# Optimization experiments

Measured on AMD Instinct MI355X. Metric: run time of the kernel, lower is better.

Reference implementation:

```python
import jax, jax.numpy as jnp
import numpy as np

B, T, D = 8, 2048, 128


def setup_inputs() -> dict:
    key = jax.random.key(0)
    kq, kk, kv = jax.random.split(key, 3)
    q = jax.random.normal(kq, (B, T, D), dtype=jnp.float32)
    k = jax.random.normal(kk, (B, T, D), dtype=jnp.float32)
    v = jax.random.normal(kv, (B, T, D), dtype=jnp.float32)
    # causal mask, broadcast over batch; 0 -> masked
    mask = jnp.tril(jnp.ones((T, T), dtype=jnp.int32))[None, :, :]
    mode = jnp.float32(0.5)  # learnable scalar parameter (init 0.5)
    return {"q": q, "k": k, "v": v, "mask": mask, "mode": mode}


def reference(q, k, v, mask, mode):
    scale = D ** (-0.5)
    # meson score: -(Q K^T) * scale
    meson = -jnp.einsum("btd,bsd->bts", q, k) * scale
    # baryon score: Q against K with feature dim rolled by 1
    k_perm = jnp.roll(k, shift=1, axis=-1)
    baryon = jnp.einsum("btd,bsd->bts", q, k_perm) * scale
    alpha = jax.nn.sigmoid(mode)
    attn = alpha * meson + (1.0 - alpha) * baryon
    attn = jnp.where(mask == 0, -jnp.inf, attn)
    attn = jax.nn.softmax(attn, axis=-1)
    return jnp.einsum("bts,bsd->btd", attn, v)
```

## Files before the change

kernel.cpp:

```cpp
#include <hip/hip_runtime.h>
#include <hip/hip_bf16.h>
#include <cstdint>
#include <cstddef>


typedef __attribute__((ext_vector_type(8))) short short8;
typedef __attribute__((ext_vector_type(4))) float f32x4;
typedef __attribute__((ext_vector_type(16))) float f32x16;
typedef __attribute__((ext_vector_type(4))) unsigned uint4v;

#define T_DIM 2048
#define D_DIM 128
#define B_DIM 8
#define SEGT 8
#define POSLOTS_PER_B 112
#define MLSLOTS_PER_B 144
#define LOG2E 1.4426950408889634f

__device__ __forceinline__ unsigned short f2bf(float f) {
  unsigned u = __builtin_bit_cast(unsigned, f);
  u += 0x7FFFu + ((u >> 16) & 1u);
  return (unsigned short)(u >> 16);
}
__device__ __forceinline__ float bf2f(unsigned short u) {
  return __uint_as_float(((unsigned)u) << 16);
}
__device__ __forceinline__ unsigned pack2bf(float a, float b) {
  return (unsigned)f2bf(a) | ((unsigned)f2bf(b) << 16);
}
__device__ __forceinline__ void gload_lds16(const void* g, void* l) {
  __builtin_amdgcn_global_load_lds(
      (const __attribute__((address_space(1))) unsigned int*)g,
      (__attribute__((address_space(3))) unsigned int*)l, 16, 0, 0);
}

__global__ __launch_bounds__(256) void prep_all(
    const float* __restrict__ q, const float* __restrict__ k, const float* __restrict__ v,
    const float* __restrict__ modep,
    unsigned short* __restrict__ qbf, unsigned short* __restrict__ kbf,
    unsigned short* __restrict__ vt)
{
  __shared__ unsigned short tile[64 * 136];
  const int b = blockIdx.x, s0 = blockIdx.y * 64;
  const int tid = threadIdx.x;
  const float alpha = 1.f / (1.f + __expf(-modep[0]));
  const float scale = 0.08838834764831845f;
  const float ca = -alpha * scale * LOG2E, cb = (1.f - alpha) * scale * LOG2E;

#pragma unroll
  for (int u = 0; u < 4; ++u) {
    int c = u * 256 + tid;
    int r = c >> 4, c8 = c & 15;
    size_t row = (size_t)b * T_DIM + s0 + r;
    float4 ka = *(const float4*)(k + row * D_DIM + c8 * 8);
    float4 kb2 = *(const float4*)(k + row * D_DIM + c8 * 8 + 4);
    short8 ko = { (short)f2bf(ka.x), (short)f2bf(ka.y), (short)f2bf(ka.z), (short)f2bf(ka.w),
                  (short)f2bf(kb2.x), (short)f2bf(kb2.y), (short)f2bf(kb2.z), (short)f2bf(kb2.w) };
    *(short8*)(kbf + row * D_DIM + c8 * 8) = ko;
    const float* qr = q + row * D_DIM;
    float e[9];
    float4 f0 = *(const float4*)(qr + c8 * 8);
    float4 f1 = *(const float4*)(qr + c8 * 8 + 4);
    e[0] = f0.x; e[1] = f0.y; e[2] = f0.z; e[3] = f0.w;
    e[4] = f1.x; e[5] = f1.y; e[6] = f1.z; e[7] = f1.w;
    e[8] = qr[(c8 * 8 + 8) & 127];
    short8 qo;
#pragma unroll
    for (int j = 0; j < 8; ++j) qo[j] = (short)f2bf(ca * e[j] + cb * e[j + 1]);
    *(short8*)(qbf + row * D_DIM + c8 * 8) = qo;
    float4 va = *(const float4*)(v + row * D_DIM + c8 * 8);
    float4 vb2 = *(const float4*)(v + row * D_DIM + c8 * 8 + 4);
    short8 vo = { (short)f2bf(va.x), (short)f2bf(va.y), (short)f2bf(va.z), (short)f2bf(va.w),
                  (short)f2bf(vb2.x), (short)f2bf(vb2.y), (short)f2bf(vb2.z), (short)f2bf(vb2.w) };
    *(short8*)(tile + r * 136 + c8 * 8) = vo;
  }
  __syncthreads();
#pragma unroll
  for (int u = 0; u < 8; ++u) {
    int c = u * 256 + tid;
    int d = c >> 4, sq = c & 15;
    ushort4 o = { tile[(sq * 4 + 0) * 136 + d], tile[(sq * 4 + 1) * 136 + d],
                  tile[(sq * 4 + 2) * 136 + d], tile[(sq * 4 + 3) * 136 + d] };
    *(ushort4*)(vt + ((size_t)b * D_DIM + d) * T_DIM + s0 + sq * 4) = o;
  }
}

__global__ __launch_bounds__(128, 2) void attn_kernel(
    const unsigned short* __restrict__ qbf, const unsigned short* __restrict__ kbf,
    const unsigned short* __restrict__ vt, float* __restrict__ out,
    unsigned short* __restrict__ po, float* __restrict__ ml)
{
  __shared__ uint4 smem4[2048];
  char* smem = (char*)smem4;
  const int tid = threadIdx.x;
  const int w = tid >> 6, lane = tid & 63;
  const int q32 = lane & 31, h = lane >> 5;
  const int b = blockIdx.x;
  const int c = 31 - (int)blockIdx.y;
  const int s = blockIdx.z;
  const int nt = 2 * c + 2;
  const int nseg = (c + 4) >> 2;
  if (s >= nseg) return;
  const int t0 = s * SEGT;
  const int t1 = min(nt, t0 + SEGT);
  const int qbw = c * 64 + w * 32;
  const int qg = qbw + q32;

  const unsigned short* kbase = kbf + (size_t)b * T_DIM * D_DIM;
  const unsigned short* vbase = vt + (size_t)b * D_DIM * T_DIM;

  short8 qf[8];
  {
    const unsigned short* qr = qbf + ((size_t)b * T_DIM + qg) * D_DIM;
#pragma unroll
    for (int j = 0; j < 8; ++j) qf[j] = *(const short8*)(qr + (2 * j + h) * 8);
  }

  f32x16 acc[4];
#pragma unroll
  for (int dt = 0; dt < 4; ++dt) acc[dt] = (f32x16)(0.f);
  float mrun = -1e30f, lsum = 0.f;

  auto stage = [&](int cur, int kt) {
    const int kv0 = kt * 32;
    char* kb = smem + cur * 8192;
    char* vb = smem + 16384 + cur * 8192;
#pragma unroll
    for (int u = 0; u < 4; ++u) {
      int s_loc = w * 16 + u * 4 + (lane >> 4);
      int slot = (lane & 15) ^ (s_loc & 15);
      gload_lds16(kbase + (size_t)(kv0 + s_loc) * D_DIM + slot * 8,
                  kb + w * 4096 + u * 1024);
    }
#pragma unroll
    for (int u = 0; u < 4; ++u) {
      int d_loc = w * 64 + u * 16 + (lane >> 2);
      int vslot = (lane & 3) ^ (d_loc & 3);
      gload_lds16(vbase + (size_t)d_loc * T_DIM + kv0 + vslot * 8,
                  vb + w * 4096 + u * 1024);
    }
  };

  stage(0, t0);
  __syncthreads();
  int cur = 0;

  for (int kt = t0; kt < t1; ++kt) {
    if (kt + 1 < t1) stage(cur ^ 1, kt + 1);
    const int kv0 = kt * 32;

    if (kv0 <= qbw + 31) {
      char* kb = smem + cur * 8192;
      char* vb = smem + 16384 + cur * 8192;

      f32x16 sj = (f32x16)(0.f);
#pragma unroll
      for (int j = 0; j < 8; ++j) {
        int r = q32;
        short8 kf = *(const short8*)(kb + r * 256 + (((2 * j + h) ^ (r & 15)) << 4));
        sj = __builtin_amdgcn_mfma_f32_32x32x16_bf16(kf, qf[j], sj, 0, 0, 0);
      }

      if (kv0 == qbw) {
#pragma unroll
        for (int r = 0; r < 16; ++r) {
          int kvg = kv0 + (r & 3) + 8 * (r >> 2) + 4 * h;
          if (kvg > qg) sj[r] = -1e30f;
        }
      }

      float lm = sj[0];
#pragma unroll
      for (int r = 1; r < 16; ++r) lm = fmaxf(lm, sj[r]);
      int ok = (lm <= mrun + 11.0f);
      if (!__all(ok)) {
        float tm = fmaxf(lm, __shfl_xor(lm, 32));
        float mnew = fmaxf(mrun, tm);
        float corr = exp2f(mrun - mnew);
        mrun = mnew;
        lsum *= corr;
#pragma unroll
        for (int dt = 0; dt < 4; ++dt) acc[dt] *= corr;
      }

      float ls = 0.f;
#pragma unroll
      for (int r = 0; r < 16; ++r) {
        float p = exp2f(sj[r] - mrun);
        sj[r] = p;
        ls += p;
      }
      lsum += ls;

      unsigned W[8];
#pragma unroll
      for (int t = 0; t < 8; ++t) W[t] = pack2bf(sj[2 * t], sj[2 * t + 1]);
      short8 pf[2];
#pragma unroll
      for (int j = 0; j < 2; ++j) {
        unsigned w0 = W[4 * j + 0], w1 = W[4 * j + 1];
        unsigned w2 = W[4 * j + 2], w3 = W[4 * j + 3];
        unsigned s0 = (unsigned)__shfl_xor((int)w0, 32);
        unsigned s1 = (unsigned)__shfl_xor((int)w1, 32);
        unsigned s2 = (unsigned)__shfl_xor((int)w2, 32);
        unsigned s3 = (unsigned)__shfl_xor((int)w3, 32);
        uint4v bw = { h ? s2 : w0, h ? s3 : w1, h ? w2 : s0, h ? w3 : s1 };
        pf[j] = __builtin_bit_cast(short8, bw);
      }

#pragma unroll
      for (int dt = 0; dt < 4; ++dt) {
        int d = dt * 32 + q32;
#pragma unroll
        for (int j = 0; j < 2; ++j) {
          short8 vf = *(const short8*)(vb + d * 64 + (((2 * j + h) ^ (d & 3)) << 4));
          acc[dt] = __builtin_amdgcn_mfma_f32_32x32x16_bf16(vf, pf[j], acc[dt], 0, 0, 0);
        }
      }
    }

    __syncthreads();
    cur ^= 1;
  }

  float lred = lsum + __shfl_xor(lsum, 32);

  if (nseg == 1) {
    float inv = 1.0f / lred;
    float* orow = out + ((size_t)b * T_DIM + qg) * D_DIM;
#pragma unroll
    for (int dt = 0; dt < 4; ++dt)
#pragma unroll
      for (int rg = 0; rg < 4; ++rg) {
        int d0 = dt * 32 + rg * 8 + 4 * h;
        f32x4 o = { acc[dt][4 * rg] * inv, acc[dt][4 * rg + 1] * inv,
                    acc[dt][4 * rg + 2] * inv, acc[dt][4 * rg + 3] * inv };
        *(f32x4*)(orow + d0) = o;
      }
  } else {
    int pofs = 0;
    for (int cc = 0; cc < c; ++cc) pofs += ((cc + 4) >> 2) - 1;
    if (s == 0) {
      float* orow = out + ((size_t)b * T_DIM + qg) * D_DIM;
#pragma unroll
      for (int dt = 0; dt < 4; ++dt)
#pragma unroll
        for (int rg = 0; rg < 4; ++rg) {
          int d0 = dt * 32 + rg * 8 + 4 * h;
          f32x4 o = { acc[dt][4 * rg], acc[dt][4 * rg + 1],
                      acc[dt][4 * rg + 2], acc[dt][4 * rg + 3] };
          *(f32x4*)(orow + d0) = o;
        }
    } else {
      unsigned short* prow = po + ((size_t)b * POSLOTS_PER_B + pofs + (s - 1)) * 8192 +
                             (w * 32 + q32) * 128;
#pragma unroll
      for (int dt = 0; dt < 4; ++dt)
#pragma unroll
        for (int rg = 0; rg < 4; ++rg) {
          int d0 = dt * 32 + rg * 8 + 4 * h;
          ushort4 o = { f2bf(acc[dt][4 * rg]), f2bf(acc[dt][4 * rg + 1]),
                        f2bf(acc[dt][4 * rg + 2]), f2bf(acc[dt][4 * rg + 3]) };
          *(ushort4*)(prow + d0) = o;
        }
    }
    if (h == 0) {
      const size_t mlslot = (size_t)b * MLSLOTS_PER_B + pofs + c + s;
      int rb = w * 32 + q32;
      ml[mlslot * 128 + rb] = mrun;
      ml[mlslot * 128 + 64 + rb] = lred;
    }
  }
}

__global__ __launch_bounds__(256) void combine_kernel(
    const unsigned short* __restrict__ po, const float* __restrict__ ml,
    float* __restrict__ out)
{
  const int tid = threadIdx.x;
  const int b = blockIdx.x;
  const int c = 4 + (int)blockIdx.y;
  const int nseg = (c + 4) >> 2;
  int pofs = 0;
  for (int cc = 0; cc < c; ++cc) pofs += ((cc + 4) >> 2) - 1;
  const size_t mlbase = (size_t)b * MLSLOTS_PER_B + pofs + c;
  const size_t pobase = (size_t)b * POSLOTS_PER_B + pofs;

  __shared__ float wgt[64][8];
  if (tid < 64) {
    float M = -1e30f;
    for (int s = 0; s < nseg; ++s)
      M = fmaxf(M, ml[(mlbase + s) * 128 + tid]);
    float L = 0.f;
    for (int s = 0; s < nseg; ++s) {
      float e = exp2f(ml[(mlbase + s) * 128 + tid] - M);
      wgt[tid][s] = e;
      L += e * ml[(mlbase + s) * 128 + 64 + tid];
    }
    float invL = 1.f / L;
    for (int s = 0; s < nseg; ++s) wgt[tid][s] *= invL;
  }
  __syncthreads();

#pragma unroll
  for (int it = 0; it < 4; ++it) {
    int vid = it * 256 + tid;
    int r = vid >> 4, ch = vid & 15;
    float* op = out + ((size_t)b * T_DIM + c * 64 + r) * D_DIM + ch * 8;
    float4 a0 = *(const float4*)op;
    float4 a1 = *(const float4*)(op + 4);
    float w0 = wgt[r][0];
    float o[8] = { w0 * a0.x, w0 * a0.y, w0 * a0.z, w0 * a0.w,
                   w0 * a1.x, w0 * a1.y, w0 * a1.z, w0 * a1.w };
    for (int s = 1; s < nseg; ++s) {
      short8 pv = *(const short8*)(po + (pobase + s - 1) * 8192 + r * 128 + ch * 8);
      float ws = wgt[r][s];
#pragma unroll
      for (int j = 0; j < 8; ++j) o[j] += ws * bf2f((unsigned short)pv[j]);
    }
    *(float4*)op = (float4){o[0], o[1], o[2], o[3]};
    *(float4*)(op + 4) = (float4){o[4], o[5], o[6], o[7]};
  }
}

extern "C" void kernel_launch(void* const* d_in, const int* in_sizes, int n_in,
                              void* d_out, int out_size, void* d_ws, size_t ws_size,
                              hipStream_t stream) {
  const float* q = (const float*)d_in[0];
  const float* k = (const float*)d_in[1];
  const float* v = (const float*)d_in[2];
  const float* mode = (const float*)d_in[4];
  float* out = (float*)d_out;

  char* ws = (char*)d_ws;
  unsigned short* qbf = (unsigned short*)(ws);
  unsigned short* kbf = (unsigned short*)(ws + 4194304);
  unsigned short* vtb = (unsigned short*)(ws + 8388608);
  unsigned short* po  = (unsigned short*)(ws + 12582912);
  float*          ml  = (float*)(ws + 27262976);

  prep_all<<<dim3(B_DIM, T_DIM / 64), 256, 0, stream>>>(q, k, v, mode, qbf, kbf, vtb);
  attn_kernel<<<dim3(B_DIM, 32, SEGT), 128, 0, stream>>>(qbf, kbf, vtb, out, po, ml);
  combine_kernel<<<dim3(B_DIM, 28), 256, 0, stream>>>(po, ml, out);
}
```

Measured before the change: 57.23 us.

## Assign one KV segment per wave with 32-row query tiles, dropping LDS staging

```diff
diff --git a/kernel.cpp b/kernel.cpp
--- a/kernel.cpp
+++ b/kernel.cpp
@@ -13,8 +13,8 @@
 #define D_DIM 128
 #define B_DIM 8
 #define SEGT 8
-#define POSLOTS_PER_B 112
-#define MLSLOTS_PER_B 144
+#define POSLOTS_PER_B 224
+#define MLSLOTS_PER_B 288
 #define LOG2E 1.4426950408889634f
 
 __device__ __forceinline__ unsigned short f2bf(float f) {
@@ -27,11 +27,6 @@
 }
 __device__ __forceinline__ unsigned pack2bf(float a, float b) {
   return (unsigned)f2bf(a) | ((unsigned)f2bf(b) << 16);
-}
-__device__ __forceinline__ void gload_lds16(const void* g, void* l) {
-  __builtin_amdgcn_global_load_lds(
-      (const __attribute__((address_space(1))) unsigned int*)g,
-      (__attribute__((address_space(3))) unsigned int*)l, 16, 0, 0);
 }
 
 __global__ __launch_bounds__(256) void prep_all(
@@ -85,26 +80,24 @@
   }
 }
 
-__global__ __launch_bounds__(128, 2) void attn_kernel(
+__global__ __launch_bounds__(256, 3) void attn_kernel(
     const unsigned short* __restrict__ qbf, const unsigned short* __restrict__ kbf,
     const unsigned short* __restrict__ vt, float* __restrict__ out,
     unsigned short* __restrict__ po, float* __restrict__ ml)
 {
-  __shared__ uint4 smem4[2048];
-  char* smem = (char*)smem4;
   const int tid = threadIdx.x;
   const int w = tid >> 6, lane = tid & 63;
   const int q32 = lane & 31, h = lane >> 5;
   const int b = blockIdx.x;
-  const int c = 31 - (int)blockIdx.y;
-  const int s = blockIdx.z;
-  const int nt = 2 * c + 2;
-  const int nseg = (c + 4) >> 2;
+  const int c = 63 - (int)blockIdx.y;
+  const int s = (int)blockIdx.z * 4 + w;
+  const int nt = c + 1;
+  const int nseg = (c + 8) >> 3;
   if (s >= nseg) return;
   const int t0 = s * SEGT;
   const int t1 = min(nt, t0 + SEGT);
-  const int qbw = c * 64 + w * 32;
-  const int qg = qbw + q32;
+  const int qb = c * 32;
+  const int qg = qb + q32;
 
   const unsigned short* kbase = kbf + (size_t)b * T_DIM * D_DIM;
   const unsigned short* vbase = vt + (size_t)b * D_DIM * T_DIM;
@@ -121,106 +114,73 @@
   for (int dt = 0; dt < 4; ++dt) acc[dt] = (f32x16)(0.f);
   float mrun = -1e30f, lsum = 0.f;
 
-  auto stage = [&](int cur, int kt) {
+  for (int kt = t0; kt < t1; ++kt) {
     const int kv0 = kt * 32;
-    char* kb = smem + cur * 8192;
-    char* vb = smem + 16384 + cur * 8192;
-#pragma unroll
-    for (int u = 0; u < 4; ++u) {
-      int s_loc = w * 16 + u * 4 + (lane >> 4);
-      int slot = (lane & 15) ^ (s_loc & 15);
-      gload_lds16(kbase + (size_t)(kv0 + s_loc) * D_DIM + slot * 8,
-                  kb + w * 4096 + u * 1024);
-    }
-#pragma unroll
-    for (int u = 0; u < 4; ++u) {
-      int d_loc = w * 64 + u * 16 + (lane >> 2);
-      int vslot = (lane & 3) ^ (d_loc & 3);
-      gload_lds16(vbase + (size_t)d_loc * T_DIM + kv0 + vslot * 8,
-                  vb + w * 4096 + u * 1024);
-    }
-  };
-
-  stage(0, t0);
-  __syncthreads();
-  int cur = 0;
-
-  for (int kt = t0; kt < t1; ++kt) {
-    if (kt + 1 < t1) stage(cur ^ 1, kt + 1);
-    const int kv0 = kt * 32;
-
-    if (kv0 <= qbw + 31) {
-      char* kb = smem + cur * 8192;
-      char* vb = smem + 16384 + cur * 8192;
-
-      f32x16 sj = (f32x16)(0.f);
-#pragma unroll
-      for (int j = 0; j < 8; ++j) {
-        int r = q32;
-        short8 kf = *(const short8*)(kb + r * 256 + (((2 * j + h) ^ (r & 15)) << 4));
-        sj = __builtin_amdgcn_mfma_f32_32x32x16_bf16(kf, qf[j], sj, 0, 0, 0);
+
+    const unsigned short* kr = kbase + (size_t)(kv0 + q32) * D_DIM;
+    f32x16 sj = (f32x16)(0.f);
+#pragma unroll
+    for (int j = 0; j < 8; ++j) {
+      short8 kf = *(const short8*)(kr + (2 * j + h) * 8);
+      sj = __builtin_amdgcn_mfma_f32_32x32x16_bf16(kf, qf[j], sj, 0, 0, 0);
+    }
+
+    if (kt == c) {
+#pragma unroll
+      for (int r = 0; r < 16; ++r) {
+        int kvg = kv0 + (r & 3) + 8 * (r >> 2) + 4 * h;
+        if (kvg > qg) sj[r] = -1e30f;
       }
-
-      if (kv0 == qbw) {
-#pragma unroll
-        for (int r = 0; r < 16; ++r) {
-          int kvg = kv0 + (r & 3) + 8 * (r >> 2) + 4 * h;
-          if (kvg > qg) sj[r] = -1e30f;
-        }
+    }
+
+    float lm = sj[0];
+#pragma unroll
+    for (int r = 1; r < 16; ++r) lm = fmaxf(lm, sj[r]);
+    int ok = (lm <= mrun + 11.0f);
+    if (!__all(ok)) {
+      float tm = fmaxf(lm, __shfl_xor(lm, 32));
+      float mnew = fmaxf(mrun, tm);
+      float corr = exp2f(mrun - mnew);
+      mrun = mnew;
+      lsum *= corr;
+#pragma unroll
+      for (int dt = 0; dt < 4; ++dt) acc[dt] *= corr;
+    }
+
+    float ls = 0.f;
+#pragma unroll
+    for (int r = 0; r < 16; ++r) {
+      float p = exp2f(sj[r] - mrun);
+      sj[r] = p;
+      ls += p;
+    }
+    lsum += ls;
+
+    unsigned W[8];
+#pragma unroll
+    for (int t = 0; t < 8; ++t) W[t] = pack2bf(sj[2 * t], sj[2 * t + 1]);
+    short8 pf[2];
+#pragma unroll
+    for (int j = 0; j < 2; ++j) {
+      unsigned w0 = W[4 * j + 0], w1 = W[4 * j + 1];
+      unsigned w2 = W[4 * j + 2], w3 = W[4 * j + 3];
+      unsigned s0 = (unsigned)__shfl_xor((int)w0, 32);
+      unsigned s1 = (unsigned)__shfl_xor((int)w1, 32);
+      unsigned s2 = (unsigned)__shfl_xor((int)w2, 32);
+      unsigned s3 = (unsigned)__shfl_xor((int)w3, 32);
+      uint4v bw = { h ? s2 : w0, h ? s3 : w1, h ? w2 : s0, h ? w3 : s1 };
+      pf[j] = __builtin_bit_cast(short8, bw);
+    }
+
+#pragma unroll
+    for (int dt = 0; dt < 4; ++dt) {
+      const unsigned short* vr = vbase + (size_t)(dt * 32 + q32) * T_DIM + kv0;
+#pragma unroll
+      for (int j = 0; j < 2; ++j) {
+        short8 vf = *(const short8*)(vr + (2 * j + h) * 8);
+        acc[dt] = __builtin_amdgcn_mfma_f32_32x32x16_bf16(vf, pf[j], acc[dt], 0, 0, 0);
       }
-
-      float lm = sj[0];
-#pragma unroll
-      for (int r = 1; r < 16; ++r) lm = fmaxf(lm, sj[r]);
-      int ok = (lm <= mrun + 11.0f);
-      if (!__all(ok)) {
-        float tm = fmaxf(lm, __shfl_xor(lm, 32));
-        float mnew = fmaxf(mrun, tm);
-        float corr = exp2f(mrun - mnew);
-        mrun = mnew;
-        lsum *= corr;
-#pragma unroll
-        for (int dt = 0; dt < 4; ++dt) acc[dt] *= corr;
-      }
-
-      float ls = 0.f;
-#pragma unroll
-      for (int r = 0; r < 16; ++r) {
-        float p = exp2f(sj[r] - mrun);
-        sj[r] = p;
-        ls += p;
-      }
-      lsum += ls;
-
-      unsigned W[8];
-#pragma unroll
-      for (int t = 0; t < 8; ++t) W[t] = pack2bf(sj[2 * t], sj[2 * t + 1]);
-      short8 pf[2];
-#pragma unroll
-      for (int j = 0; j < 2; ++j) {
-        unsigned w0 = W[4 * j + 0], w1 = W[4 * j + 1];
-        unsigned w2 = W[4 * j + 2], w3 = W[4 * j + 3];
-        unsigned s0 = (unsigned)__shfl_xor((int)w0, 32);
-        unsigned s1 = (unsigned)__shfl_xor((int)w1, 32);
-        unsigned s2 = (unsigned)__shfl_xor((int)w2, 32);
-        unsigned s3 = (unsigned)__shfl_xor((int)w3, 32);
-        uint4v bw = { h ? s2 : w0, h ? s3 : w1, h ? w2 : s0, h ? w3 : s1 };
-        pf[j] = __builtin_bit_cast(short8, bw);
-      }
-
-#pragma unroll
-      for (int dt = 0; dt < 4; ++dt) {
-        int d = dt * 32 + q32;
-#pragma unroll
-        for (int j = 0; j < 2; ++j) {
-          short8 vf = *(const short8*)(vb + d * 64 + (((2 * j + h) ^ (d & 3)) << 4));
-          acc[dt] = __builtin_amdgcn_mfma_f32_32x32x16_bf16(vf, pf[j], acc[dt], 0, 0, 0);
-        }
-      }
-    }
-
-    __syncthreads();
-    cur ^= 1;
+    }
   }
 
   float lred = lsum + __shfl_xor(lsum, 32);
@@ -239,7 +199,7 @@
       }
   } else {
     int pofs = 0;
-    for (int cc = 0; cc < c; ++cc) pofs += ((cc + 4) >> 2) - 1;
+    for (int cc = 0; cc < c; ++cc) pofs += ((cc + SEGT) >> 3) - 1;
     if (s == 0) {
       float* orow = out + ((size_t)b * T_DIM + qg) * D_DIM;
 #pragma unroll
@@ -252,8 +212,8 @@
           *(f32x4*)(orow + d0) = o;
         }
     } else {
-      unsigned short* prow = po + ((size_t)b * POSLOTS_PER_B + pofs + (s - 1)) * 8192 +
-                             (w * 32 + q32) * 128;
+      unsigned short* prow = po + ((size_t)b * POSLOTS_PER_B + pofs + (s - 1)) * 4096 +
+                             q32 * 128;
 #pragma unroll
       for (int dt = 0; dt < 4; ++dt)
 #pragma unroll
@@ -266,9 +226,8 @@
     }
     if (h == 0) {
       const size_t mlslot = (size_t)b * MLSLOTS_PER_B + pofs + c + s;
-      int rb = w * 32 + q32;
-      ml[mlslot * 128 + rb] = mrun;
-      ml[mlslot * 128 + 64 + rb] = lred;
+      ml[mlslot * 64 + q32] = mrun;
+      ml[mlslot * 64 + 32 + q32] = lred;
     }
   }
 }
@@ -279,23 +238,24 @@
 {
   const int tid = threadIdx.x;
   const int b = blockIdx.x;
-  const int c = 4 + (int)blockIdx.y;
-  const int nseg = (c + 4) >> 2;
+  const int c = SEGT + (int)blockIdx.y;
+  const int nt = c + 1;
+  const int nseg = (nt + SEGT - 1) >> 3;
   int pofs = 0;
-  for (int cc = 0; cc < c; ++cc) pofs += ((cc + 4) >> 2) - 1;
+  for (int cc = 0; cc < c; ++cc) pofs += ((cc + SEGT) >> 3) - 1;
   const size_t mlbase = (size_t)b * MLSLOTS_PER_B + pofs + c;
   const size_t pobase = (size_t)b * POSLOTS_PER_B + pofs;
 
-  __shared__ float wgt[64][8];
-  if (tid < 64) {
+  __shared__ float wgt[32][8];
+  if (tid < 32) {
     float M = -1e30f;
     for (int s = 0; s < nseg; ++s)
-      M = fmaxf(M, ml[(mlbase + s) * 128 + tid]);
+      M = fmaxf(M, ml[(mlbase + s) * 64 + tid]);
     float L = 0.f;
     for (int s = 0; s < nseg; ++s) {
-      float e = exp2f(ml[(mlbase + s) * 128 + tid] - M);
+      float e = exp2f(ml[(mlbase + s) * 64 + tid] - M);
       wgt[tid][s] = e;
-      L += e * ml[(mlbase + s) * 128 + 64 + tid];
+      L += e * ml[(mlbase + s) * 64 + 32 + tid];
     }
     float invL = 1.f / L;
     for (int s = 0; s < nseg; ++s) wgt[tid][s] *= invL;
@@ -303,17 +263,17 @@
   __syncthreads();
 
 #pragma unroll
-  for (int it = 0; it < 4; ++it) {
+  for (int it = 0; it < 2; ++it) {
     int vid = it * 256 + tid;
     int r = vid >> 4, ch = vid & 15;
-    float* op = out + ((size_t)b * T_DIM + c * 64 + r) * D_DIM + ch * 8;
+    float* op = out + ((size_t)b * T_DIM + c * 32 + r) * D_DIM + ch * 8;
     float4 a0 = *(const float4*)op;
     float4 a1 = *(const float4*)(op + 4);
     float w0 = wgt[r][0];
     float o[8] = { w0 * a0.x, w0 * a0.y, w0 * a0.z, w0 * a0.w,
                    w0 * a1.x, w0 * a1.y, w0 * a1.z, w0 * a1.w };
     for (int s = 1; s < nseg; ++s) {
-      short8 pv = *(const short8*)(po + (pobase + s - 1) * 8192 + r * 128 + ch * 8);
+      short8 pv = *(const short8*)(po + (pobase + s - 1) * 4096 + r * 128 + ch * 8);
       float ws = wgt[r][s];
 #pragma unroll
       for (int j = 0; j < 8; ++j) o[j] += ws * bf2f((unsigned short)pv[j]);
@@ -340,6 +300,6 @@
   float*          ml  = (float*)(ws + 27262976);
 
   prep_all<<<dim3(B_DIM, T_DIM / 64), 256, 0, stream>>>(q, k, v, mode, qbf, kbf, vtb);
-  attn_kernel<<<dim3(B_DIM, 32, SEGT), 128, 0, stream>>>(qbf, kbf, vtb, out, po, ml);
-  combine_kernel<<<dim3(B_DIM, 28), 256, 0, stream>>>(po, ml, out);
-}
+  attn_kernel<<<dim3(B_DIM, 64, 2), 256, 0, stream>>>(qbf, kbf, vtb, out, po, ml);
+  combine_kernel<<<dim3(B_DIM, 64 - SEGT), 256, 0, stream>>>(po, ml, out);
+}
```

Result: slower. 76.77 us (+34.1%).
